# Kernel optimization log

Measured on AMD Instinct MI355X. Metric: run time of the kernel, lower is better.

Reference implementation:

```python
import jax, jax.numpy as jnp
import numpy as np

NF = 64      # feature channels
DG = 8       # deformable groups
K = 9        # 3x3 kernel taps


def conv3(x, w, b):
    # 3x3 conv, stride 1, pad 1, NCHW/OIHW
    y = jax.lax.conv_general_dilated(x, w, (1, 1), ((1, 1), (1, 1)),
                                     dimension_numbers=('NCHW', 'OIHW', 'NCHW'))
    return y + b[None, :, None, None]


def lrelu(x):
    return jnp.where(x >= 0, x, 0.1 * x)


def up2(x):
    # matches F.interpolate(scale_factor=2, mode='bilinear', align_corners=False)
    b, c, h, w = x.shape
    return jax.image.resize(x, (b, c, 2 * h, 2 * w), method='bilinear')


def _sample_group(img, py, px):
    # img: [Cg,H,W]; py,px: [K,H,W] absolute float sample coords; zero pad outside
    H, W = img.shape[-2:]
    y0 = jnp.floor(py)
    x0 = jnp.floor(px)
    wy = py - y0
    wx = px - x0
    y0i = y0.astype(jnp.int32)
    x0i = x0.astype(jnp.int32)

    def gather(yi, xi):
        valid = (yi >= 0) & (yi < H) & (xi >= 0) & (xi < W)
        yc = jnp.clip(yi, 0, H - 1)
        xc = jnp.clip(xi, 0, W - 1)
        return img[:, yc, xc] * valid[None].astype(img.dtype)  # [Cg,K,H,W]

    v00 = gather(y0i, x0i)
    v01 = gather(y0i, x0i + 1)
    v10 = gather(y0i + 1, x0i)
    v11 = gather(y0i + 1, x0i + 1)
    return (1 - wy) * ((1 - wx) * v00 + wx * v01) + wy * ((1 - wx) * v10 + wx * v11)


def dcn_sep(x, off_fea, om_w, om_b, w, b):
    # DCN_sep: conv_offset_mask(off_fea) -> (o1,o2,mask); modulated deformable 3x3 conv on x
    B, C, H, W = x.shape
    om = conv3(off_fea, om_w, om_b)                       # [B, 3*DG*K, H, W]
    o1, o2, m = jnp.split(om, 3, axis=1)
    off_y = o1.reshape(B, DG, K, H, W)
    off_x = o2.reshape(B, DG, K, H, W)
    mask = jax.nn.sigmoid(m).reshape(B, DG, K, H, W)

    k = jnp.arange(3, dtype=x.dtype) - 1.0
    dy = jnp.repeat(k, 3)   # [K] row-major kernel offsets
    dx = jnp.tile(k, 3)
    hh = jnp.arange(H, dtype=x.dtype)
    ww = jnp.arange(W, dtype=x.dtype)
    py = off_y + dy[:, None, None] + hh[None, :, None]    # [B,DG,K,H,W]
    px = off_x + dx[:, None, None] + ww[None, None, :]

    xg = x.reshape(B, DG, C // DG, H, W)
    samp = jax.vmap(jax.vmap(_sample_group))(xg, py, px)  # [B,DG,Cg,K,H,W]
    samp = (samp * mask[:, :, None]).reshape(B, C, K, H, W)
    wk = w.reshape(w.shape[0], C, K)                      # [O,C,9]
    return jnp.einsum('ock,bckhw->bohw', wk, samp) + b[None, :, None, None]


def setup_inputs() -> dict:
    key = jax.random.key(0)
    ks = jax.random.split(key, 16)
    d = {
        'fea1_l1': jax.random.normal(ks[0], (4, NF, 128, 128), jnp.float32),
        'fea1_l2': jax.random.normal(ks[1], (4, NF, 64, 64), jnp.float32),
        'fea1_l3': jax.random.normal(ks[2], (4, NF, 32, 32), jnp.float32),
        'fea2_l1': jax.random.normal(ks[3], (4, NF, 128, 128), jnp.float32),
        'fea2_l2': jax.random.normal(ks[4], (4, NF, 64, 64), jnp.float32),
        'fea2_l3': jax.random.normal(ks[5], (4, NF, 32, 32), jnp.float32),
        # 8 plain 3x3 convs with in=2*nf: [L3_off1, L2_off1, L2_off2, L2_fea, L1_off1, L1_off2, L1_fea, cas_off1]
        'w128': jax.random.normal(ks[6], (8, NF, 2 * NF, 3, 3), jnp.float32) * 0.05,
        'b128': jax.random.normal(ks[7], (8, NF), jnp.float32) * 0.01,
        # 4 plain 3x3 convs with in=nf: [L3_off2, L2_off3, L1_off3, cas_off2]
        'w64': jax.random.normal(ks[8], (4, NF, NF, 3, 3), jnp.float32) * 0.05,
        'b64': jax.random.normal(ks[9], (4, NF), jnp.float32) * 0.01,
        # 4 DCN_sep modules: [L3, L2, L1, cas]
        'om_w': jax.random.normal(ks[10], (4, 3 * DG * K, NF, 3, 3), jnp.float32) * 0.01,
        'om_b': jax.random.normal(ks[11], (4, 3 * DG * K), jnp.float32) * 0.01,
        'dcn_w': jax.random.normal(ks[12], (4, NF, NF, 3, 3), jnp.float32) * 0.05,
        'dcn_b': jax.random.normal(ks[13], (4, NF), jnp.float32) * 0.01,
    }
    return d


def reference(fea1_l1, fea1_l2, fea1_l3, fea2_l1, fea2_l2, fea2_l3,
              w128, b128, w64, b64, om_w, om_b, dcn_w, dcn_b):
    cat = lambda a, b_: jnp.concatenate([a, b_], axis=1)
    # L3
    L3_off = lrelu(conv3(cat(fea1_l3, fea2_l3), w128[0], b128[0]))
    L3_off = lrelu(conv3(L3_off, w64[0], b64[0]))
    L3_fea = lrelu(dcn_sep(fea1_l3, L3_off, om_w[0], om_b[0], dcn_w[0], dcn_b[0]))
    # L2
    L2_off = lrelu(conv3(cat(fea1_l2, fea2_l2), w128[1], b128[1]))
    L3_off_up = up2(L3_off)
    L2_off = lrelu(conv3(cat(L2_off, L3_off_up * 2), w128[2], b128[2]))
    L2_off = lrelu(conv3(L2_off, w64[1], b64[1]))
    L2_fea = dcn_sep(fea1_l2, L2_off, om_w[1], om_b[1], dcn_w[1], dcn_b[1])
    L3_fea_up = up2(L3_fea)
    L2_fea = lrelu(conv3(cat(L2_fea, L3_fea_up), w128[3], b128[3]))
    # L1
    L1_off = lrelu(conv3(cat(fea1_l1, fea2_l1), w128[4], b128[4]))
    L2_off_up = up2(L2_off)
    L1_off = lrelu(conv3(cat(L1_off, L2_off_up * 2), w128[5], b128[5]))
    L1_off = lrelu(conv3(L1_off, w64[2], b64[2]))
    L1_fea = dcn_sep(fea1_l1, L1_off, om_w[2], om_b[2], dcn_w[2], dcn_b[2])
    L2_fea_up = up2(L2_fea)
    L1_fea = conv3(cat(L1_fea, L2_fea_up), w128[6], b128[6])
    # Cascading
    off = lrelu(conv3(cat(L1_fea, fea2_l1), w128[7], b128[7]))
    off = lrelu(conv3(off, w64[3], b64[3]))
    return lrelu(dcn_sep(L1_fea, off, om_w[3], om_b[3], dcn_w[3], dcn_b[3]))
```

## Files before the change

kernel.cpp:

```cpp
#include <hip/hip_runtime.h>
#include <cstdint>
#include <cstddef>


__global__ void transpose_convw(const float* __restrict__ w, float* __restrict__ wt,
                                int OC, int C, long total)
{
    long i = (long)blockIdx.x * 256 + threadIdx.x;
    if (i >= total) return;
    const int per = OC * C * 9;
    int n  = (int)(i / per);
    int r  = (int)(i - (long)n * per);
    int o  = r / (C * 9);
    int r2 = r - o * (C * 9);
    wt[(long)n * per + (long)r2 * OC + o] = w[i];
}

__global__ void transpose_dcnw(const float* __restrict__ w, float* __restrict__ wt, long total)
{
    long i = (long)blockIdx.x * 256 + threadIdx.x;
    if (i >= total) return;
    int n = (int)(i / 36864);
    int r = (int)(i % 36864);
    int o = r / 576;
    int c = (r % 576) / 9;
    int k = r % 9;
    wt[(long)n * 36864 + ((size_t)k * 64 + c) * 64 + o] = w[i];
}

template<int C1, int C2, int OCPW, bool RELU>
__global__ __launch_bounds__(256)
void conv3x3_k(const float* __restrict__ in1, const float* __restrict__ in2,
               float scale2, const float* __restrict__ WT, const float* __restrict__ bg,
               float* __restrict__ out, int H, int W, int OCtot, int nChunk)
{
    constexpr int C = C1 + C2;
    const int bz = blockIdx.z;
    const int b = bz / nChunk, chunk = bz - b * nChunk;
    const int tid = threadIdx.x;
    const int wid = __builtin_amdgcn_readfirstlane(tid >> 6);
    const int p  = tid & 63;
    const int py = p >> 3, px = p & 7;
    const int h0 = blockIdx.y * 8, w0 = blockIdx.x * 8;
    const size_t HW = (size_t)H * W;
    const int ocbase = chunk * (4 * OCPW) + wid * OCPW;

    __shared__ float tile[8][10][11];

    float acc[OCPW];
#pragma unroll
    for (int o = 0; o < OCPW; ++o) acc[o] = 0.f;

    for (int c0 = 0; c0 < C; c0 += 8) {
        __syncthreads();
        for (int i = tid; i < 800; i += 256) {
            int cc = i / 100, r = i - cc * 100;
            int yy = r / 10, xx = r - yy * 10;
            int gy = h0 + yy - 1, gx = w0 + xx - 1;
            int c = c0 + cc;
            float v = 0.f;
            if (gy >= 0 && gy < H && gx >= 0 && gx < W) {
                if (C2 == 0 || c < C1)
                    v = in1[((size_t)b * C1 + c) * HW + (size_t)gy * W + gx];
                else
                    v = in2[((size_t)b * C2 + (c - C1)) * HW + (size_t)gy * W + gx] * scale2;
            }
            tile[cc][yy][xx] = v;
        }
        __syncthreads();

#pragma unroll
        for (int cc = 0; cc < 8; ++cc) {
            float v[9];
#pragma unroll
            for (int dy = 0; dy < 3; ++dy)
#pragma unroll
                for (int dx = 0; dx < 3; ++dx)
                    v[dy * 3 + dx] = tile[cc][py + dy][px + dx];
            const float* wp = WT + ((size_t)(c0 + cc) * 9) * OCtot + ocbase;
#pragma unroll
            for (int k = 0; k < 9; ++k) {
                const float* wk = wp + (size_t)k * OCtot;
#pragma unroll
                for (int o = 0; o < OCPW; ++o)
                    acc[o] = fmaf(wk[o], v[k], acc[o]);
            }
        }
    }

    const int h = h0 + py, w = w0 + px;
    float* op = out + ((size_t)b * OCtot + ocbase) * HW + (size_t)h * W + w;
#pragma unroll
    for (int o = 0; o < OCPW; ++o) {
        float r = acc[o] + bg[ocbase + o];
        if (RELU) r = (r >= 0.f) ? r : 0.1f * r;
        op[(size_t)o * HW] = r;
    }
}

template<bool RELU>
__global__ __launch_bounds__(256)
void dcn_k(const float* __restrict__ x, const float* __restrict__ om,
           const float* __restrict__ Wt, const float* __restrict__ bg,
           float* __restrict__ out, int H, int W)
{
    const int b = blockIdx.z;
    const int tid = threadIdx.x;
    const int wid = __builtin_amdgcn_readfirstlane(tid >> 6);
    const int p = tid & 63;
    const int h = blockIdx.y * 8 + (p >> 3), w = blockIdx.x * 8 + (p & 7);
    const size_t HW = (size_t)H * W;

    float acc[64];
#pragma unroll
    for (int o = 0; o < 64; ++o) acc[o] = 0.f;

    const float* omb = om + (size_t)b * 216 * HW + (size_t)h * W + w;
    const float* xb  = x + (size_t)b * 64 * HW;

    for (int gg = 0; gg < 2; ++gg) {
        const int g = wid * 2 + gg;
        for (int k = 0; k < 9; ++k) {
            const int ch = g * 9 + k;
            float oy = omb[(size_t)ch * HW];
            float ox = omb[(size_t)(72 + ch) * HW];
            float mr = omb[(size_t)(144 + ch) * HW];
            float m  = 1.f / (1.f + expf(-mr));

            float pyf = oy + (float)(k / 3 - 1) + (float)h;
            float pxf = ox + (float)(k % 3 - 1) + (float)w;
            float fy = floorf(pyf), fx = floorf(pxf);
            float wy = pyf - fy, wx = pxf - fx;
            int y0 = (int)fy, x0 = (int)fx;
            int y1 = y0 + 1, x1 = x0 + 1;
            bool vy0 = (y0 >= 0) & (y0 < H), vy1 = (y1 >= 0) & (y1 < H);
            bool vx0 = (x0 >= 0) & (x0 < W), vx1 = (x1 >= 0) & (x1 < W);
            int y0c = y0 < 0 ? 0 : (y0 >= H ? H - 1 : y0);
            int y1c = y1 < 0 ? 0 : (y1 >= H ? H - 1 : y1);
            int x0c = x0 < 0 ? 0 : (x0 >= W ? W - 1 : x0);
            int x1c = x1 < 0 ? 0 : (x1 >= W ? W - 1 : x1);
            float w00 = (1.f - wy) * (1.f - wx) * m * ((vy0 & vx0) ? 1.f : 0.f);
            float w01 = (1.f - wy) * wx         * m * ((vy0 & vx1) ? 1.f : 0.f);
            float w10 = wy         * (1.f - wx) * m * ((vy1 & vx0) ? 1.f : 0.f);
            float w11 = wy         * wx         * m * ((vy1 & vx1) ? 1.f : 0.f);
            size_t i00 = (size_t)y0c * W + x0c, i01 = (size_t)y0c * W + x1c;
            size_t i10 = (size_t)y1c * W + x0c, i11 = (size_t)y1c * W + x1c;

            float s[8];
#pragma unroll
            for (int cg = 0; cg < 8; ++cg) {
                const float* xc = xb + (size_t)(g * 8 + cg) * HW;
                s[cg] = w00 * xc[i00] + w01 * xc[i01] + w10 * xc[i10] + w11 * xc[i11];
            }
#pragma unroll
            for (int cg = 0; cg < 8; ++cg) {
                const float* wko = Wt + ((size_t)k * 64 + g * 8 + cg) * 64;
                float sv = s[cg];
#pragma unroll
                for (int o = 0; o < 64; ++o)
                    acc[o] = fmaf(wko[o], sv, acc[o]);
            }
        }
    }

    __shared__ float red[3][64][65];
    if (wid > 0) {
#pragma unroll
        for (int o = 0; o < 64; ++o) red[wid - 1][p][o] = acc[o];
    }
    __syncthreads();
    if (wid == 0) {
#pragma unroll
        for (int o = 0; o < 64; ++o)
            acc[o] += red[0][p][o] + red[1][p][o] + red[2][p][o];
        float* op = out + ((size_t)b * 64) * HW + (size_t)h * W + w;
#pragma unroll
        for (int o = 0; o < 64; ++o) {
            float r = acc[o] + bg[o];
            if (RELU) r = (r >= 0.f) ? r : 0.1f * r;
            op[(size_t)o * HW] = r;
        }
    }
}

__global__ void up2_k(const float* __restrict__ in, float* __restrict__ out,
                      int H, int W, long total)
{
    long idx = (long)blockIdx.x * 256 + threadIdx.x;
    if (idx >= total) return;
    const int W2 = 2 * W, H2 = 2 * H;
    int w2 = (int)(idx % W2);
    long t = idx / W2;
    int h2 = (int)(t % H2);
    long bc = t / H2;
    const float* src = in + bc * (size_t)H * W;
    int jx = w2 >> 1, jy = h2 >> 1;
    int x0, y0; float wx0, wy0;
    if (w2 & 1) { x0 = jx;     wx0 = 0.75f; } else { x0 = jx - 1; wx0 = 0.25f; }
    if (h2 & 1) { y0 = jy;     wy0 = 0.75f; } else { y0 = jy - 1; wy0 = 0.25f; }
    int x1 = x0 + 1 > W - 1 ? W - 1 : x0 + 1;
    int y1 = y0 + 1 > H - 1 ? H - 1 : y0 + 1;
    if (x0 < 0) x0 = 0;
    if (y0 < 0) y0 = 0;
    float v00 = src[(size_t)y0 * W + x0], v01 = src[(size_t)y0 * W + x1];
    float v10 = src[(size_t)y1 * W + x0], v11 = src[(size_t)y1 * W + x1];
    float wx1 = 1.f - wx0, wy1 = 1.f - wy0;
    out[idx] = wy0 * (wx0 * v00 + wx1 * v01) + wy1 * (wx0 * v10 + wx1 * v11);
}

extern "C" void kernel_launch(void* const* d_in, const int* in_sizes, int n_in,
                              void* d_out, int out_size, void* d_ws, size_t ws_size,
                              hipStream_t stream)
{
    const float* fea1_l1 = (const float*)d_in[0];
    const float* fea1_l2 = (const float*)d_in[1];
    const float* fea1_l3 = (const float*)d_in[2];
    const float* fea2_l1 = (const float*)d_in[3];
    const float* fea2_l2 = (const float*)d_in[4];
    const float* fea2_l3 = (const float*)d_in[5];
    const float* w128  = (const float*)d_in[6];
    const float* b128  = (const float*)d_in[7];
    const float* w64   = (const float*)d_in[8];
    const float* b64   = (const float*)d_in[9];
    const float* om_w  = (const float*)d_in[10];
    const float* om_b  = (const float*)d_in[11];
    const float* dcn_w = (const float*)d_in[12];
    const float* dcn_b = (const float*)d_in[13];
    float* outp = (float*)d_out;

    float* ws = (float*)d_ws;
    const size_t S1  = (size_t)4 * 64 * 128 * 128;
    const size_t S2  = (size_t)4 * 64 * 64 * 64;
    const size_t S3  = (size_t)4 * 64 * 32 * 32;
    const size_t ASZ = (size_t)4 * 216 * 128 * 128;
    float* A  = ws;
    float* Bb = ws + S1;
    float* Cb = ws + 2 * S1;
    float* Db = ws + 3 * S1;
    float* sA = ws + 4 * S1;
    float* sG = sA + ASZ - 2 * S2;
    float* sH = sA + ASZ - S2;
    float* dT = sA + ASZ;

    float* w128T = outp;
    float* w64T  = outp + 589824;
    float* omwT  = outp + 737280;

    float* e3a = A;            float* e3b = A + S3;       float* e3c = A + 2 * S3;
    float* f2a = Bb;           float* f2b = Bb + S2;      float* f2c = Bb + 2 * S2;

    const dim3 blk(256);

    transpose_convw<<<(int)((8l*64*128*9 + 255) / 256), 256, 0, stream>>>(w128, w128T, 64, 128, 8l*64*128*9);
    transpose_convw<<<(int)((4l*64*64*9  + 255) / 256), 256, 0, stream>>>(w64,  w64T,  64, 64,  4l*64*64*9);
    transpose_convw<<<(int)((4l*216*64*9 + 255) / 256), 256, 0, stream>>>(om_w, omwT, 216, 64,  4l*216*64*9);
    transpose_dcnw <<<(int)((4l*36864    + 255) / 256), 256, 0, stream>>>(dcn_w, dT, 4l*36864);

    conv3x3_k<64,64,16,true ><<<dim3(4,4,4),  blk, 0, stream>>>(fea1_l3, fea2_l3, 1.f, w128T + 0*73728, b128 + 0*64, e3a, 32, 32, 64, 1);
    conv3x3_k<64, 0,16,true ><<<dim3(4,4,4),  blk, 0, stream>>>(e3a, nullptr, 1.f, w64T + 0*36864, b64 + 0*64, e3b, 32, 32, 64, 1);
    conv3x3_k<64, 0,27,false><<<dim3(4,4,8),  blk, 0, stream>>>(e3b, nullptr, 1.f, omwT + 0*124416, om_b + 0*216, sA, 32, 32, 216, 2);
    dcn_k<true ><<<dim3(4,4,4), blk, 0, stream>>>(fea1_l3, sA, dT + 0*36864, dcn_b + 0*64, e3c, 32, 32);

    conv3x3_k<64,64,16,true ><<<dim3(8,8,4),  blk, 0, stream>>>(fea1_l2, fea2_l2, 1.f, w128T + 1*73728, b128 + 1*64, f2a, 64, 64, 64, 1);
    up2_k<<<(int)((S2 + 255) / 256), 256, 0, stream>>>(e3b, f2b, 32, 32, (long)S2);
    conv3x3_k<64,64,16,true ><<<dim3(8,8,4),  blk, 0, stream>>>(f2a, f2b, 2.f, w128T + 2*73728, b128 + 2*64, f2c, 64, 64, 64, 1);
    conv3x3_k<64, 0,16,true ><<<dim3(8,8,4),  blk, 0, stream>>>(f2c, nullptr, 1.f, w64T + 1*36864, b64 + 1*64, sG, 64, 64, 64, 1);
    conv3x3_k<64, 0,27,false><<<dim3(8,8,8),  blk, 0, stream>>>(sG, nullptr, 1.f, omwT + 1*124416, om_b + 1*216, sA, 64, 64, 216, 2);
    dcn_k<false><<<dim3(8,8,4), blk, 0, stream>>>(fea1_l2, sA, dT + 1*36864, dcn_b + 1*64, f2a, 64, 64);
    up2_k<<<(int)((S2 + 255) / 256), 256, 0, stream>>>(e3c, f2b, 32, 32, (long)S2);
    conv3x3_k<64,64,16,true ><<<dim3(8,8,4),  blk, 0, stream>>>(f2a, f2b, 1.f, w128T + 3*73728, b128 + 3*64, sH, 64, 64, 64, 1);

    conv3x3_k<64,64,16,true ><<<dim3(16,16,4), blk, 0, stream>>>(fea1_l1, fea2_l1, 1.f, w128T + 4*73728, b128 + 4*64, A, 128, 128, 64, 1);
    up2_k<<<(int)((S1 + 255) / 256), 256, 0, stream>>>(sG, Bb, 64, 64, (long)S1);
    conv3x3_k<64,64,16,true ><<<dim3(16,16,4), blk, 0, stream>>>(A, Bb, 2.f, w128T + 5*73728, b128 + 5*64, Cb, 128, 128, 64, 1);
    conv3x3_k<64, 0,16,true ><<<dim3(16,16,4), blk, 0, stream>>>(Cb, nullptr, 1.f, w64T + 2*36864, b64 + 2*64, A, 128, 128, 64, 1);
    up2_k<<<(int)((S1 + 255) / 256), 256, 0, stream>>>(sH, Bb, 64, 64, (long)S1);
    conv3x3_k<64, 0,27,false><<<dim3(16,16,8), blk, 0, stream>>>(A, nullptr, 1.f, omwT + 2*124416, om_b + 2*216, sA, 128, 128, 216, 2);
    dcn_k<false><<<dim3(16,16,4), blk, 0, stream>>>(fea1_l1, sA, dT + 2*36864, dcn_b + 2*64, Cb, 128, 128);
    conv3x3_k<64,64,16,false><<<dim3(16,16,4), blk, 0, stream>>>(Cb, Bb, 1.f, w128T + 6*73728, b128 + 6*64, Db, 128, 128, 64, 1);

    conv3x3_k<64,64,16,true ><<<dim3(16,16,4), blk, 0, stream>>>(Db, fea2_l1, 1.f, w128T + 7*73728, b128 + 7*64, A, 128, 128, 64, 1);
    conv3x3_k<64, 0,16,true ><<<dim3(16,16,4), blk, 0, stream>>>(A, nullptr, 1.f, w64T + 3*36864, b64 + 3*64, Bb, 128, 128, 64, 1);
    conv3x3_k<64, 0,27,false><<<dim3(16,16,8), blk, 0, stream>>>(Bb, nullptr, 1.f, omwT + 3*124416, om_b + 3*216, sA, 128, 128, 216, 2);
    dcn_k<true ><<<dim3(16,16,4), blk, 0, stream>>>(Db, sA, dT + 3*36864, dcn_b + 3*64, outp, 128, 128);
}
```

Before: 2.940 ms.

## Run 3x3 convolutions on bf16 MFMA with split hi/lo precision compensation

Replaces the scalar FP32 direct 3x3 convolution with an implicit-GEMM kernel using 16x16x32 bf16 MFMA instructions. Inputs and weights are each split into high and low bf16 parts, and three MFMAs per tile approximate FP32 accuracy. Input tiles are staged in LDS as channel-packed bf16 vectors, and weights are pre-transposed into a tap-major, padded-OC layout. This moves the dominant conv FLOPs from vector ALUs to matrix cores, at the cost of extra conversion work and a small accuracy loss from dropping the lo*lo term.

```diff
diff --git a/kernel.cpp b/kernel.cpp
--- a/kernel.cpp
+++ b/kernel.cpp
@@ -3,17 +3,28 @@
 #include <cstddef>
 
 
-__global__ void transpose_convw(const float* __restrict__ w, float* __restrict__ wt,
-                                int OC, int C, long total)
-{
+typedef __bf16 bf16x8 __attribute__((ext_vector_type(8)));
+typedef float  f32x4  __attribute__((ext_vector_type(4)));
+
+template<int OCPAD, int C>
+__global__ void wsplit_k(const float* __restrict__ src, __bf16* __restrict__ dst,
+                         int OC, long total)
+{
+    const int per = 9 * OCPAD * C;
     long i = (long)blockIdx.x * 256 + threadIdx.x;
     if (i >= total) return;
-    const int per = OC * C * 9;
     int n  = (int)(i / per);
     int r  = (int)(i - (long)n * per);
-    int o  = r / (C * 9);
-    int r2 = r - o * (C * 9);
-    wt[(long)n * per + (long)r2 * OC + o] = w[i];
+    int t  = r / (OCPAD * C);
+    int r2 = r - t * (OCPAD * C);
+    int o  = r2 / C;
+    int c  = r2 - o * C;
+    float v = (o < OC) ? src[(((long)n * OC + o) * C + c) * 9 + t] : 0.f;
+    __bf16 h = (__bf16)v;
+    __bf16 l = (__bf16)(v - (float)h);
+    __bf16* d = dst + (long)n * 2 * per;
+    d[r]       = h;
+    d[per + r] = l;
 }
 
 __global__ void transpose_dcnw(const float* __restrict__ w, float* __restrict__ wt, long total)
@@ -28,73 +39,96 @@
     wt[(long)n * 36864 + ((size_t)k * 64 + c) * 64 + o] = w[i];
 }
 
-template<int C1, int C2, int OCPW, bool RELU>
+template<int C1, int C2, int NMT, int OCPAD, bool RELU>
 __global__ __launch_bounds__(256)
-void conv3x3_k(const float* __restrict__ in1, const float* __restrict__ in2,
-               float scale2, const float* __restrict__ WT, const float* __restrict__ bg,
-               float* __restrict__ out, int H, int W, int OCtot, int nChunk)
+void conv_mfma_k(const float* __restrict__ in1, const float* __restrict__ in2,
+                 float scale2, const __bf16* __restrict__ wt, const float* __restrict__ bg,
+                 float* __restrict__ out, int H, int W, int OCtot)
 {
     constexpr int C = C1 + C2;
+    constexpr int PER = 9 * OCPAD * C;
+    constexpr int NCHUNK = OCPAD / (NMT * 16);
     const int bz = blockIdx.z;
-    const int b = bz / nChunk, chunk = bz - b * nChunk;
+    const int b = bz / NCHUNK, chunk = bz - b * NCHUNK;
+    const int ocblk = chunk * NMT * 16;
     const int tid = threadIdx.x;
     const int wid = __builtin_amdgcn_readfirstlane(tid >> 6);
-    const int p  = tid & 63;
-    const int py = p >> 3, px = p & 7;
+    const int lane = tid & 63;
+    const int pix = lane & 15;
+    const int oct = lane >> 4;
     const int h0 = blockIdx.y * 8, w0 = blockIdx.x * 8;
     const size_t HW = (size_t)H * W;
-    const int ocbase = chunk * (4 * OCPW) + wid * OCPW;
-
-    __shared__ float tile[8][10][11];
-
-    float acc[OCPW];
-#pragma unroll
-    for (int o = 0; o < OCPW; ++o) acc[o] = 0.f;
-
-    for (int c0 = 0; c0 < C; c0 += 8) {
+
+    __shared__ __bf16 XH[100 * 40];
+    __shared__ __bf16 XL[100 * 40];
+
+    f32x4 accm[NMT], accc[NMT];
+#pragma unroll
+    for (int mt = 0; mt < NMT; ++mt) { accm[mt] = f32x4{0,0,0,0}; accc[mt] = f32x4{0,0,0,0}; }
+
+    const int py = 2 * wid + (pix >> 3), px = pix & 7;
+    const int pixbase = (py * 10 + px) * 40 + oct * 8;
+    const int alane = (lane & 15) * C + oct * 8;
+
+    for (int c0 = 0; c0 < C; c0 += 32) {
         __syncthreads();
-        for (int i = tid; i < 800; i += 256) {
-            int cc = i / 100, r = i - cc * 100;
-            int yy = r / 10, xx = r - yy * 10;
-            int gy = h0 + yy - 1, gx = w0 + xx - 1;
-            int c = c0 + cc;
-            float v = 0.f;
-            if (gy >= 0 && gy < H && gx >= 0 && gx < W) {
-                if (C2 == 0 || c < C1)
-                    v = in1[((size_t)b * C1 + c) * HW + (size_t)gy * W + gx];
-                else
-                    v = in2[((size_t)b * C2 + (c - C1)) * HW + (size_t)gy * W + gx] * scale2;
-            }
-            tile[cc][yy][xx] = v;
+        for (int task = tid; task < 400; task += 256) {
+            int p  = task >> 2, o8 = (task & 3) * 8;
+            int y  = p / 10, x = p - y * 10;
+            int gy = h0 + y - 1, gx = w0 + x - 1;
+            bool valid = (gy >= 0) & (gy < H) & (gx >= 0) & (gx < W);
+            int cc = c0 + o8;
+            const float* src; float sc;
+            if (C2 == 0 || cc < C1) { src = in1 + ((size_t)b * C1 + cc) * HW; sc = 1.f; }
+            else                    { src = in2 + ((size_t)b * C2 + (cc - C1)) * HW; sc = scale2; }
+            const size_t gofs = (size_t)gy * W + gx;
+            bf16x8 hv, lv;
+#pragma unroll
+            for (int j = 0; j < 8; ++j) {
+                float v = valid ? src[(size_t)j * HW + gofs] * sc : 0.f;
+                __bf16 h = (__bf16)v;
+                hv[j] = h;
+                lv[j] = (__bf16)(v - (float)h);
+            }
+            *(bf16x8*)(&XH[p * 40 + o8]) = hv;
+            *(bf16x8*)(&XL[p * 40 + o8]) = lv;
         }
         __syncthreads();
 
 #pragma unroll
-        for (int cc = 0; cc < 8; ++cc) {
-            float v[9];
-#pragma unroll
-            for (int dy = 0; dy < 3; ++dy)
-#pragma unroll
-                for (int dx = 0; dx < 3; ++dx)
-                    v[dy * 3 + dx] = tile[cc][py + dy][px + dx];
-            const float* wp = WT + ((size_t)(c0 + cc) * 9) * OCtot + ocbase;
-#pragma unroll
-            for (int k = 0; k < 9; ++k) {
-                const float* wk = wp + (size_t)k * OCtot;
-#pragma unroll
-                for (int o = 0; o < OCPW; ++o)
-                    acc[o] = fmaf(wk[o], v[k], acc[o]);
-            }
-        }
-    }
-
-    const int h = h0 + py, w = w0 + px;
-    float* op = out + ((size_t)b * OCtot + ocbase) * HW + (size_t)h * W + w;
-#pragma unroll
-    for (int o = 0; o < OCPW; ++o) {
-        float r = acc[o] + bg[ocbase + o];
-        if (RELU) r = (r >= 0.f) ? r : 0.1f * r;
-        op[(size_t)o * HW] = r;
+        for (int dy = 0; dy < 3; ++dy) {
+#pragma unroll
+            for (int dx = 0; dx < 3; ++dx) {
+                const int t = dy * 3 + dx;
+                const int loff = pixbase + (dy * 10 + dx) * 40;
+                bf16x8 bh = *(const bf16x8*)(&XH[loff]);
+                bf16x8 bl = *(const bf16x8*)(&XL[loff]);
+                const __bf16* wbase = wt + (size_t)(t * OCPAD + ocblk) * C + c0 + alane;
+#pragma unroll
+                for (int mt = 0; mt < NMT; ++mt) {
+                    bf16x8 ah = *(const bf16x8*)(wbase + mt * 16 * C);
+                    bf16x8 al = *(const bf16x8*)(wbase + mt * 16 * C + PER);
+                    accm[mt] = __builtin_amdgcn_mfma_f32_16x16x32_bf16(ah, bh, accm[mt], 0, 0, 0);
+                    accc[mt] = __builtin_amdgcn_mfma_f32_16x16x32_bf16(ah, bl, accc[mt], 0, 0, 0);
+                    accc[mt] = __builtin_amdgcn_mfma_f32_16x16x32_bf16(al, bh, accc[mt], 0, 0, 0);
+                }
+            }
+        }
+    }
+
+    const int orow4 = oct * 4;
+    float* obase = out + (size_t)b * OCtot * HW + (size_t)(h0 + py) * W + (w0 + px);
+#pragma unroll
+    for (int mt = 0; mt < NMT; ++mt) {
+#pragma unroll
+        for (int j = 0; j < 4; ++j) {
+            int oc = ocblk + mt * 16 + orow4 + j;
+            if (oc < OCtot) {
+                float r = accm[mt][j] + accc[mt][j] + bg[oc];
+                if (RELU) r = (r >= 0.f) ? r : 0.1f * r;
+                obase[(size_t)oc * HW] = r;
+            }
+        }
     }
 }
 
@@ -242,45 +276,51 @@
     float* sH = sA + ASZ - S2;
     float* dT = sA + ASZ;
 
-    float* w128T = outp;
-    float* w64T  = outp + 589824;
-    float* omwT  = outp + 737280;
-
-    float* e3a = A;            float* e3b = A + S3;       float* e3c = A + 2 * S3;
-    float* f2a = Bb;           float* f2b = Bb + S2;      float* f2c = Bb + 2 * S2;
+    __bf16* U = (__bf16*)d_out;
+    __bf16* w128T = U;
+    __bf16* w64T  = U + 1179648;
+    __bf16* omT   = U + 1474560;
+
+    float* e3a = A;   float* e3b = A + S3;   float* e3c = A + 2 * S3;
+    float* f2a = Bb;  float* f2b = Bb + S2;  float* f2c = Bb + 2 * S2;
 
     const dim3 blk(256);
 
-    transpose_convw<<<(int)((8l*64*128*9 + 255) / 256), 256, 0, stream>>>(w128, w128T, 64, 128, 8l*64*128*9);
-    transpose_convw<<<(int)((4l*64*64*9  + 255) / 256), 256, 0, stream>>>(w64,  w64T,  64, 64,  4l*64*64*9);
-    transpose_convw<<<(int)((4l*216*64*9 + 255) / 256), 256, 0, stream>>>(om_w, omwT, 216, 64,  4l*216*64*9);
-    transpose_dcnw <<<(int)((4l*36864    + 255) / 256), 256, 0, stream>>>(dcn_w, dT, 4l*36864);
-
-    conv3x3_k<64,64,16,true ><<<dim3(4,4,4),  blk, 0, stream>>>(fea1_l3, fea2_l3, 1.f, w128T + 0*73728, b128 + 0*64, e3a, 32, 32, 64, 1);
-    conv3x3_k<64, 0,16,true ><<<dim3(4,4,4),  blk, 0, stream>>>(e3a, nullptr, 1.f, w64T + 0*36864, b64 + 0*64, e3b, 32, 32, 64, 1);
-    conv3x3_k<64, 0,27,false><<<dim3(4,4,8),  blk, 0, stream>>>(e3b, nullptr, 1.f, omwT + 0*124416, om_b + 0*216, sA, 32, 32, 216, 2);
+    {
+        long t1 = 8l * 73728;
+        wsplit_k<64,128><<<(int)((t1 + 255) / 256), 256, 0, stream>>>(w128, w128T, 64, t1);
+        long t2 = 4l * 36864;
+        wsplit_k<64,64><<<(int)((t2 + 255) / 256), 256, 0, stream>>>(w64, w64T, 64, t2);
+        long t3 = 4l * 129024;
+        wsplit_k<224,64><<<(int)((t3 + 255) / 256), 256, 0, stream>>>(om_w, omT, 216, t3);
+        transpose_dcnw<<<(int)((4l * 36864 + 255) / 256), 256, 0, stream>>>(dcn_w, dT, 4l * 36864);
+    }
+
+    conv_mfma_k<64,64,4,64,true ><<<dim3(4,4,4), blk, 0, stream>>>(fea1_l3, fea2_l3, 1.f, w128T + 0l*147456, b128 + 0*64, e3a, 32, 32, 64);
+    conv_mfma_k<64, 0,4,64,true ><<<dim3(4,4,4), blk, 0, stream>>>(e3a, nullptr, 1.f, w64T + 0l*73728, b64 + 0*64, e3b, 32, 32, 64);
+    conv_mfma_k<64, 0,7,224,false><<<dim3(4,4,8), blk, 0, stream>>>(e3b, nullptr, 1.f, omT + 0l*258048, om_b + 0*216, sA, 32, 32, 216);
     dcn_k<true ><<<dim3(4,4,4), blk, 0, stream>>>(fea1_l3, sA, dT + 0*36864, dcn_b + 0*64, e3c, 32, 32);
 
-    conv3x3_k<64,64,16,true ><<<dim3(8,8,4),  blk, 0, stream>>>(fea1_l2, fea2_l2, 1.f, w128T + 1*73728, b128 + 1*64, f2a, 64, 64, 64, 1);
+    conv_mfma_k<64,64,4,64,true ><<<dim3(8,8,4), blk, 0, stream>>>(fea1_l2, fea2_l2, 1.f, w128T + 1l*147456, b128 + 1*64, f2a, 64, 64, 64);
     up2_k<<<(int)((S2 + 255) / 256), 256, 0, stream>>>(e3b, f2b, 32, 32, (long)S2);
-    conv3x3_k<64,64,16,true ><<<dim3(8,8,4),  blk, 0, stream>>>(f2a, f2b, 2.f, w128T + 2*73728, b128 + 2*64, f2c, 64, 64, 64, 1);
-    conv3x3_k<64, 0,16,true ><<<dim3(8,8,4),  blk, 0, stream>>>(f2c, nullptr, 1.f, w64T + 1*36864, b64 + 1*64, sG, 64, 64, 64, 1);
-    conv3x3_k<64, 0,27,false><<<dim3(8,8,8),  blk, 0, stream>>>(sG, nullptr, 1.f, omwT + 1*124416, om_b + 1*216, sA, 64, 64, 216, 2);
+    conv_mfma_k<64,64,4,64,true ><<<dim3(8,8,4), blk, 0, stream>>>(f2a, f2b, 2.f, w128T + 2l*147456, b128 + 2*64, f2c, 64, 64, 64);
+    conv_mfma_k<64, 0,4,64,true ><<<dim3(8,8,4), blk, 0, stream>>>(f2c, nullptr, 1.f, w64T + 1l*73728, b64 + 1*64, sG, 64, 64, 64);
+    conv_mfma_k<64, 0,7,224,false><<<dim3(8,8,8), blk, 0, stream>>>(sG, nullptr, 1.f, omT + 1l*258048, om_b + 1*216, sA, 64, 64, 216);
     dcn_k<false><<<dim3(8,8,4), blk, 0, stream>>>(fea1_l2, sA, dT + 1*36864, dcn_b + 1*64, f2a, 64, 64);
     up2_k<<<(int)((S2 + 255) / 256), 256, 0, stream>>>(e3c, f2b, 32, 32, (long)S2);
-    conv3x3_k<64,64,16,true ><<<dim3(8,8,4),  blk, 0, stream>>>(f2a, f2b, 1.f, w128T + 3*73728, b128 + 3*64, sH, 64, 64, 64, 1);
-
-    conv3x3_k<64,64,16,true ><<<dim3(16,16,4), blk, 0, stream>>>(fea1_l1, fea2_l1, 1.f, w128T + 4*73728, b128 + 4*64, A, 128, 128, 64, 1);
+    conv_mfma_k<64,64,4,64,true ><<<dim3(8,8,4), blk, 0, stream>>>(f2a, f2b, 1.f, w128T + 3l*147456, b128 + 3*64, sH, 64, 64, 64);
+
+    conv_mfma_k<64,64,4,64,true ><<<dim3(16,16,4), blk, 0, stream>>>(fea1_l1, fea2_l1, 1.f, w128T + 4l*147456, b128 + 4*64, A, 128, 128, 64);
     up2_k<<<(int)((S1 + 255) / 256), 256, 0, stream>>>(sG, Bb, 64, 64, (long)S1);
-    conv3x3_k<64,64,16,true ><<<dim3(16,16,4), blk, 0, stream>>>(A, Bb, 2.f, w128T + 5*73728, b128 + 5*64, Cb, 128, 128, 64, 1);
-    conv3x3_k<64, 0,16,true ><<<dim3(16,16,4), blk, 0, stream>>>(Cb, nullptr, 1.f, w64T + 2*36864, b64 + 2*64, A, 128, 128, 64, 1);
+    conv_mfma_k<64,64,4,64,true ><<<dim3(16,16,4), blk, 0, stream>>>(A, Bb, 2.f, w128T + 5l*147456, b128 + 5*64, Cb, 128, 128, 64);
+    conv_mfma_k<64, 0,4,64,true ><<<dim3(16,16,4), blk, 0, stream>>>(Cb, nullptr, 1.f, w64T + 2l*73728, b64 + 2*64, A, 128, 128, 64);
     up2_k<<<(int)((S1 + 255) / 256), 256, 0, stream>>>(sH, Bb, 64, 64, (long)S1);
-    conv3x3_k<64, 0,27,false><<<dim3(16,16,8), blk, 0, stream>>>(A, nullptr, 1.f, omwT + 2*124416, om_b + 2*216, sA, 128, 128, 216, 2);
+    conv_mfma_k<64, 0,7,224,false><<<dim3(16,16,8), blk, 0, stream>>>(A, nullptr, 1.f, omT + 2l*258048, om_b + 2*216, sA, 128, 128, 216);
     dcn_k<false><<<dim3(16,16,4), blk, 0, stream>>>(fea1_l1, sA, dT + 2*36864, dcn_b + 2*64, Cb, 128, 128);
-    conv3x3_k<64,64,16,false><<<dim3(16,16,4), blk, 0, stream>>>(Cb, Bb, 1.f, w128T + 6*73728, b128 + 6*64, Db, 128, 128, 64, 1);
-
-    conv3x3_k<64,64,16,true ><<<dim3(16,16,4), blk, 0, stream>>>(Db, fea2_l1, 1.f, w128T + 7*73728, b128 + 7*64, A, 128, 128, 64, 1);
-    conv3x3_k<64, 0,16,true ><<<dim3(16,16,4), blk, 0, stream>>>(A, nullptr, 1.f, w64T + 3*36864, b64 + 3*64, Bb, 128, 128, 64, 1);
-    conv3x3_k<64, 0,27,false><<<dim3(16,16,8), blk, 0, stream>>>(Bb, nullptr, 1.f, omwT + 3*124416, om_b + 3*216, sA, 128, 128, 216, 2);
+    conv_mfma_k<64,64,4,64,false><<<dim3(16,16,4), blk, 0, stream>>>(Cb, Bb, 1.f, w128T + 6l*147456, b128 + 6*64, Db, 128, 128, 64);
+
+    conv_mfma_k<64,64,4,64,true ><<<dim3(16,16,4), blk, 0, stream>>>(Db, fea2_l1, 1.f, w128T + 7l*147456, b128 + 7*64, A, 128, 128, 64);
+    conv_mfma_k<64, 0,4,64,true ><<<dim3(16,16,4), blk, 0, stream>>>(A, nullptr, 1.f, w64T + 3l*73728, b64 + 3*64, Bb, 128, 128, 64);
+    conv_mfma_k<64, 0,7,224,false><<<dim3(16,16,8), blk, 0, stream>>>(Bb, nullptr, 1.f, omT + 3l*258048, om_b + 3*216, sA, 128, 128, 216);
     dcn_k<true ><<<dim3(16,16,4), blk, 0, stream>>>(Db, sA, dT + 3*36864, dcn_b + 3*64, outp, 128, 128);
 }
```

Result: faster. 2.438 ms (-17.0%).
